# Performance work log

Hardware: AMD Instinct MI355X
Metric: run time of the kernel (lower is better)

Reference implementation:

```python
import jax, jax.numpy as jnp
import numpy as np

N = 30000; E = 480000; B = 32
IN_H = 129; IN_P = 15; HID = 64; HEADS = 8; OUT = 129


def gat_conv(x, src, dst, edge_attr, W, a_src, a_dst, We, a_e, bias, concat):
    # PyG GATConv with edge_dim, add_self_loops=True (fill_value='mean'), negative_slope=0.2
    n = x.shape[0]
    H, C = a_src.shape
    ones = jnp.ones((src.shape[0],), x.dtype)
    deg = jax.ops.segment_sum(ones, dst, num_segments=n)
    ea_mean = jax.ops.segment_sum(edge_attr, dst, num_segments=n) / jnp.clip(deg, 1.0)[:, None]
    loop = jnp.arange(n, dtype=src.dtype)
    s = jnp.concatenate([src, loop])
    t = jnp.concatenate([dst, loop])
    ea = jnp.concatenate([edge_attr, ea_mean], axis=0)
    xw = (x @ W).reshape(n, H, C)              # [N,H,C]
    a_s = jnp.sum(xw * a_src, axis=-1)         # [N,H]
    a_d = jnp.sum(xw * a_dst, axis=-1)         # [N,H]
    ew = (ea @ We).reshape(-1, H, C)           # [E2,H,C]
    a_ed = jnp.sum(ew * a_e, axis=-1)          # [E2,H]
    alpha = jax.nn.leaky_relu(a_s[s] + a_d[t] + a_ed, 0.2)
    amax = jax.ops.segment_max(alpha, t, num_segments=n)   # every node has a self-loop
    expa = jnp.exp(alpha - amax[t])
    denom = jax.ops.segment_sum(expa, t, num_segments=n)
    alpha = expa / denom[t]                    # segment softmax over dst
    out = jax.ops.segment_sum(xw[s] * alpha[..., None], t, num_segments=n)  # [N,H,C]
    out = out.reshape(n, H * C) if concat else jnp.mean(out, axis=1)
    return out + bias


def setup_inputs():
    key = jax.random.key(0)
    ks = jax.random.split(key, 40)
    g = lambda k, s: (jax.random.normal(k, s, jnp.float32) * (1.0 / np.sqrt(s[0])))
    d = {}
    d['x_hrtf'] = jax.random.normal(ks[0], (N, IN_H), jnp.float32)
    d['x_pos'] = jax.random.normal(ks[1], (N, IN_P), jnp.float32)
    d['edge_attr_hrtf'] = jax.random.normal(ks[2], (E, 1), jnp.float32)
    d['edge_attr_pos'] = jax.random.normal(ks[3], (E, 1), jnp.float32)
    # hrtf branch, layer 1 (heads=8, concat)
    d['W1h'] = g(ks[4], (IN_H, HEADS * HID)); d['as1h'] = g(ks[5], (HEADS, HID)); d['ad1h'] = g(ks[6], (HEADS, HID))
    d['We1h'] = g(ks[7], (1, HEADS * HID)); d['ae1h'] = g(ks[8], (HEADS, HID)); d['b1h'] = jnp.zeros((HEADS * HID,), jnp.float32)
    # hrtf branch, layer 2 (heads=1, mean)
    d['W2h'] = g(ks[9], (HEADS * HID, OUT)); d['as2h'] = g(ks[10], (1, OUT)); d['ad2h'] = g(ks[11], (1, OUT))
    d['We2h'] = g(ks[12], (1, OUT)); d['ae2h'] = g(ks[13], (1, OUT)); d['b2h'] = jnp.zeros((OUT,), jnp.float32)
    # pos branch, layer 1
    d['W1p'] = g(ks[14], (IN_P, HEADS * HID)); d['as1p'] = g(ks[15], (HEADS, HID)); d['ad1p'] = g(ks[16], (HEADS, HID))
    d['We1p'] = g(ks[17], (1, HEADS * HID)); d['ae1p'] = g(ks[18], (HEADS, HID)); d['b1p'] = jnp.zeros((HEADS * HID,), jnp.float32)
    # pos branch, layer 2
    d['W2p'] = g(ks[19], (HEADS * HID, OUT)); d['as2p'] = g(ks[20], (1, OUT)); d['ad2p'] = g(ks[21], (1, OUT))
    d['We2p'] = g(ks[22], (1, OUT)); d['ae2p'] = g(ks[23], (1, OUT)); d['b2p'] = jnp.zeros((OUT,), jnp.float32)
    # final fc
    d['Wfc'] = g(ks[24], (2 * OUT, 129)); d['bfc'] = jnp.zeros((129,), jnp.float32)
    d['edge_index_hrtf'] = jax.random.randint(ks[25], (2, E), 0, N, jnp.int32)
    d['edge_index_pos'] = jax.random.randint(ks[26], (2, E), 0, N, jnp.int32)
    d['batch'] = ((jnp.arange(N) * B) // N).astype(jnp.int32)  # sorted, equal-sized graphs
    d['num_graphs'] = B
    return d


def reference(x_hrtf, x_pos, edge_attr_hrtf, edge_attr_pos, W1h, as1h, ad1h, We1h, ae1h, b1h, W2h, as2h, ad2h, We2h, ae2h, b2h, W1p, as1p, ad1p, We1p, ae1p, b1p, W2p, as2p, ad2p, We2p, ae2p, b2p, Wfc, bfc, edge_index_hrtf, edge_index_pos, batch, num_graphs):
    sh, th = edge_index_hrtf[0], edge_index_hrtf[1]
    sp, tp = edge_index_pos[0], edge_index_pos[1]
    h = jax.nn.elu(gat_conv(x_hrtf, sh, th, edge_attr_hrtf, W1h, as1h, ad1h, We1h, ae1h, b1h, True))
    h = gat_conv(h, sh, th, edge_attr_hrtf, W2h, as2h, ad2h, We2h, ae2h, b2h, False)
    p = jax.nn.elu(gat_conv(x_pos, sp, tp, edge_attr_pos, W1p, as1p, ad1p, We1p, ae1p, b1p, True))
    p = gat_conv(p, sp, tp, edge_attr_pos, W2p, as2p, ad2p, We2p, ae2p, b2p, False)
    counts = jax.ops.segment_sum(jnp.ones_like(batch), batch, num_segments=num_graphs)
    last = jnp.cumsum(counts) - 1              # last node index of each graph
    z = jnp.concatenate([h[last], p[last]], axis=-1)
    z = z @ Wfc + bfc
    return z[:, None, :]                       # [B,1,129]
```

## Files before the change

### kernel.cpp

```cpp
#include <hip/hip_runtime.h>

#define N_NODES 30000
#define N_EDGES 480000
#define NB      32
#define HEADS   8
#define F1      512
#define OUT_C   129
#define OUT_S   132
#define W1TS    132

#define CAP1   1024
#define MAXD   64
#define NZREG  (8 + 2 * CAP1 + 2 * NB)

#define SHIFT1 12.0f
#define SHIFT2 20.0f

__device__ __forceinline__ float lrelu(float a) { return a > 0.f ? a : 0.2f * a; }

__device__ __forceinline__ int graph_of(int v) { return (int)(((unsigned)v * 2u) / 1875u); }
__device__ __forceinline__ int last_of(int b) { return (int)((((unsigned)(b + 1) * 1875u) + 1u) / 2u) - 1; }
__device__ __forceinline__ bool is_last_node(int v) { return v == last_of(graph_of(v)); }

__global__ void k_prep(const float* We1h, const float* ae1h,
                       const float* We1p, const float* ae1p,
                       const float* We2h, const float* ae2h,
                       const float* We2p, const float* ae2p,
                       const float* __restrict__ W1h, const float* __restrict__ W1p,
                       const float* as1h, const float* as1p,
                       const float* ad1h, const float* ad1p,
                       float* k12, float* __restrict__ w_as, float* __restrict__ w_ad,
                       int* __restrict__ zreg, int* __restrict__ inv1) {
    int gid = blockIdx.x * 256 + threadIdx.x;
    if (gid < 15000) ((int4*)inv1)[gid] = make_int4(-1, -1, -1, -1);
    if (gid < NZREG) zreg[gid] = 0;
    if (blockIdx.x == 0) {
        int t = threadIdx.x;
        if (t < 8) {
            float s = 0.f;
            for (int c = 0; c < 64; c++) s += We1h[t * 64 + c] * ae1h[t * 64 + c];
            k12[t] = s;
        } else if (t < 16) {
            int h = t - 8;
            float s = 0.f;
            for (int c = 0; c < 64; c++) s += We1p[h * 64 + c] * ae1p[h * 64 + c];
            k12[8 + h] = s;
        } else if (t == 16) {
            float s = 0.f;
            for (int c = 0; c < OUT_C; c++) s += We2h[c] * ae2h[c];
            k12[16] = s;
        } else if (t == 17) {
            float s = 0.f;
            for (int c = 0; c < OUT_C; c++) s += We2p[c] * ae2p[c];
            k12[17] = s;
        }
    }
    if (blockIdx.x >= 64 && blockIdx.x < 96) {
        int bb = blockIdx.x - 64;
        int br = bb >> 4, type = (bb >> 3) & 1, h = bb & 7;
        const float* W1 = br ? W1p : W1h;
        const float* a  = type ? (br ? ad1p : ad1h) : (br ? as1p : as1h);
        float* outp = (type ? w_ad : w_as) + (size_t)(br * 8 + h) * W1TS;
        int K = br ? 15 : 129;
        int d = threadIdx.x;
        if (d < K) {
            float s = 0.f;
            for (int c = 0; c < 64; c++) s += W1[(size_t)d * F1 + h * 64 + c] * a[h * 64 + c];
            outp[d] = s;
        }
    }
}

__global__ __launch_bounds__(256) void k_scan2(const int* __restrict__ ei_h,
        const int* __restrict__ ei_p, const float* __restrict__ ea_h,
        const float* __restrict__ ea_p, int* inv1,
        int* degcnt2, int* eb2v, float* eb2e) {
    int br = blockIdx.y;
    const int* ei = br ? ei_p : ei_h;
    const float* ea = br ? ea_p : ea_h;
    const int* src = ei; const int* dst = ei + N_EDGES;
    inv1 += br * N_NODES;
    degcnt2 += br * NB; eb2v += br * NB * MAXD; eb2e += br * NB * MAXD;
    int tid = threadIdx.x;
    if (blockIdx.x == 0 && tid < NB) inv1[last_of(tid)] = -2;
    int base = (blockIdx.x * 256 + tid) * 4;
    if (base >= N_EDGES) return;
    int4 d = *(const int4*)(dst + base);
    int dv[4] = {d.x, d.y, d.z, d.w};
#pragma unroll
    for (int q = 0; q < 4; q++) {
        if (is_last_node(dv[q])) {
            int e = base + q;
            int b = graph_of(dv[q]);
            int slot = atomicAdd(degcnt2 + b, 1);
            if (slot < MAXD) { eb2v[b * MAXD + slot] = src[e]; eb2e[b * MAXD + slot] = ea[e]; }
            inv1[src[e]] = -2;
        }
    }
}

__global__ __launch_bounds__(256) void k_compact1(int* inv1, int* nodes1, int* cnt) {
    __shared__ int s_v[256];
    __shared__ int s_n, s_base;
    int br = blockIdx.y;
    inv1 += br * N_NODES; nodes1 += br * CAP1;
    int* cntp = cnt + br * 4 + 0;
    int tid = threadIdx.x;
    if (tid == 0) s_n = 0;
    __syncthreads();
    int base = (blockIdx.x * 256 + tid) * 4;
    if (base < N_NODES) {
        int4 w = *(const int4*)(inv1 + base);
        int vv[4] = {w.x, w.y, w.z, w.w};
#pragma unroll
        for (int q = 0; q < 4; q++) {
            if (vv[q] == -2) {
                int p = atomicAdd(&s_n, 1);
                if (p < 256) s_v[p] = base + q;
            }
        }
    }
    __syncthreads();
    int n = s_n; if (n > 256) n = 256;
    if (tid == 0) s_base = atomicAdd(cntp, n);
    __syncthreads();
    for (int q = tid; q < n; q += 256) {
        int j = s_base + q;
        if (j < CAP1) { inv1[s_v[q]] = j; nodes1[j] = s_v[q]; }
    }
}

__global__ __launch_bounds__(256) void k_scan1(const int* __restrict__ ei_h,
        const int* __restrict__ ei_p, const float* __restrict__ ea_h,
        const float* __restrict__ ea_p, const int* __restrict__ inv1,
        int* degcnt1, int* ebv1, float* ebe1) {
    int br = blockIdx.y;
    const int* ei = br ? ei_p : ei_h;
    const float* ea = br ? ea_p : ea_h;
    const int* src = ei; const int* dst = ei + N_EDGES;
    inv1 += br * N_NODES;
    degcnt1 += br * CAP1; ebv1 += (size_t)br * CAP1 * MAXD; ebe1 += (size_t)br * CAP1 * MAXD;
    int tid = threadIdx.x;
    int base = (blockIdx.x * 256 + tid) * 4;
    if (base >= N_EDGES) return;
    int4 d = *(const int4*)(dst + base);
    int dv[4] = {d.x, d.y, d.z, d.w};
#pragma unroll
    for (int q = 0; q < 4; q++) {
        int jj = inv1[dv[q]];
        if (jj >= 0) {
            int e = base + q;
            int slot = atomicAdd(degcnt1 + jj, 1);
            if (slot < MAXD) { ebv1[jj * MAXD + slot] = src[e]; ebe1[jj * MAXD + slot] = ea[e]; }
        }
    }
}

__global__ __launch_bounds__(256) void k_agg1x(const int* __restrict__ ebv1,
        const float* __restrict__ ebe1, const int* __restrict__ degcnt1,
        const int* __restrict__ nodes1, const int* cnt,
        const float* __restrict__ x_h, const float* __restrict__ x_p,
        const float* __restrict__ w_as, const float* __restrict__ w_ad,
        const float* __restrict__ k12, const float* __restrict__ b1h,
        const float* __restrict__ b1p, const float* __restrict__ W1h,
        const float* __restrict__ W1p, const float* __restrict__ W2h,
        const float* __restrict__ W2p, const float* __restrict__ as2h,
        const float* __restrict__ as2p, const float* __restrict__ ad2h,
        const float* __restrict__ ad2p,
        float* __restrict__ xw2, float* __restrict__ as2v, float* __restrict__ ad2all) {
    __shared__ float s_x[MAXD + 9][W1TS];
    __shared__ int   s_v[MAXD + 1];
    __shared__ float s_e[MAXD + 1];
    __shared__ float s_ex[(MAXD + 1) * 8];
    __shared__ float s_den[8];
    __shared__ float s_adh[8];
    __shared__ float s_k1[8];
    __shared__ float s_h1[F1];
    __shared__ float s_row[OUT_S];
    int br = blockIdx.y;
    const float* x    = br ? x_p : x_h;
    const float* b1   = br ? b1p : b1h;
    const float* W1   = br ? W1p : W1h;
    const float* W2   = br ? W2p : W2h;
    const float* as2w = br ? as2p : as2h;
    const float* ad2w = br ? ad2p : ad2h;
    const float* wasb = w_as + (size_t)br * 8 * W1TS;
    const float* wadb = w_ad + (size_t)br * 8 * W1TS;
    int K = br ? 15 : 129;
    int n1 = cnt[br * 4 + 0]; if (n1 > CAP1) n1 = CAP1;
    int j = blockIdx.x;
    if (j >= n1) return;
    int tid = threadIdx.x;
    int deg = degcnt1[br * CAP1 + j]; if (deg > MAXD) deg = MAXD;
    const int*   ebv = ebv1 + ((size_t)br * CAP1 + j) * MAXD;
    const float* ebe = ebe1 + ((size_t)br * CAP1 + j) * MAXD;
    if (tid < deg) { s_v[tid] = ebv[tid]; s_e[tid] = ebe[tid]; }
    if (tid == 0) s_v[deg] = nodes1[br * CAP1 + j];
    if (tid >= 72 && tid < 80) s_k1[tid - 72] = k12[br * 8 + (tid - 72)];
    __syncthreads();
    int total = deg + 1;
    for (int k = tid >> 6; k < total; k += 4) {
        const float* xr = x + (size_t)s_v[k] * K;
        for (int d = (tid & 63); d < K; d += 64) s_x[k][d] = xr[d];
    }
    __syncthreads();
    if (tid < 64) {
        float part = (tid < deg) ? s_e[tid] : 0.f;
#pragma unroll
        for (int o = 32; o > 0; o >>= 1) part += __shfl_down(part, o);
        if (tid == 0) s_e[deg] = part / fmaxf((float)deg, 1.f);
    }
    for (int t = tid; t < total * 8 + 8; t += 256) {
        int k, h; const float* wv;
        if (t < total * 8) { k = t >> 3; h = t & 7; wv = wasb + (size_t)h * W1TS; }
        else               { k = deg; h = t - total * 8; wv = wadb + (size_t)h * W1TS; }
        float dot = 0.f;
        for (int d = 0; d < K; d++) dot += s_x[k][d] * wv[d];
        if (t < total * 8) s_ex[t] = dot; else s_adh[h] = dot;
    }
    __syncthreads();
    for (int t = tid; t < total * 8; t += 256) {
        int k = t >> 3, h = t & 7;
        float a = lrelu(s_ex[t] + s_adh[h] + s_e[k] * s_k1[h]);
        s_ex[t] = __expf(a - SHIFT1);
    }
    __syncthreads();
    if (tid >= 192 && tid < 200) {
        int h = tid - 192;
        float d = 0.f;
        for (int k = 0; k < total; k++) d += s_ex[k * 8 + h];
        s_den[h] = d;
    }
    if (tid < K) {
        float acc[8];
#pragma unroll
        for (int h = 0; h < 8; h++) acc[h] = 0.f;
        for (int k = 0; k < total; k++) {
            float xv = s_x[k][tid];
#pragma unroll
            for (int h = 0; h < 8; h++) acc[h] += s_ex[k * 8 + h] * xv;
        }
#pragma unroll
        for (int h = 0; h < 8; h++) s_x[MAXD + 1 + h][tid] = acc[h];
    }
    __syncthreads();
    {
        int h0 = tid >> 6, h1i = h0 + 4;
        float a0 = 0.f, a1 = 0.f;
        for (int d = 0; d < K; d++) {
            float xa0 = s_x[MAXD + 1 + h0][d];
            float xa1 = s_x[MAXD + 1 + h1i][d];
            a0 += xa0 * W1[(size_t)d * F1 + tid];
            a1 += xa1 * W1[(size_t)d * F1 + tid + 256];
        }
        float v0 = a0 / s_den[h0] + b1[tid];
        float v1 = a1 / s_den[h1i] + b1[tid + 256];
        s_h1[tid]       = v0 > 0.f ? v0 : (__expf(v0) - 1.f);
        s_h1[tid + 256] = v1 > 0.f ? v1 : (__expf(v1) - 1.f);
    }
    __syncthreads();
    if (tid < OUT_C) {
        float a = 0.f;
        for (int k = 0; k < F1; k++) a += s_h1[k] * W2[(size_t)k * OUT_C + tid];
        s_row[tid] = a;
        xw2[((size_t)br * CAP1 + j) * OUT_S + tid] = a;
    }
    __syncthreads();
    if (tid < 128) {
        int w = tid >> 6, l = tid & 63;
        const float* av = w ? ad2w : as2w;
        float p = s_row[l] * av[l] + s_row[64 + l] * av[64 + l];
        if (l == 0) p += s_row[128] * av[128];
#pragma unroll
        for (int o = 32; o > 0; o >>= 1) p += __shfl_down(p, o);
        if (l == 0) {
            if (w) ad2all[br * CAP1 + j] = p;
            else   as2v[br * CAP1 + j] = p;
        }
    }
}

__global__ __launch_bounds__(256) void k_agg2fc(const int* __restrict__ eb2v,
        const float* __restrict__ eb2e, const int* __restrict__ degcnt2,
        const int* __restrict__ inv1, const int* cnt,
        const float* __restrict__ as2v, const float* __restrict__ ad2all,
        const float* __restrict__ k12, const float* __restrict__ b2h,
        const float* __restrict__ b2p, const float* __restrict__ xw2,
        const float* __restrict__ Wfc, const float* __restrict__ bfc,
        float* __restrict__ out) {
    __shared__ int   s_j[MAXD + 1];
    __shared__ float s_e[MAXD + 1];
    __shared__ float s_ex[MAXD + 1];
    __shared__ float s_den;
    __shared__ float hcat[2 * OUT_C];
    int b = blockIdx.x;
    int tid = threadIdx.x;
    for (int br = 0; br < 2; br++) {
        const float* b2 = br ? b2p : b2h;
        const int* inv1b = inv1 + br * N_NODES;
        const float* as2vb = as2v + br * CAP1;
        const float* ad2b = ad2all + br * CAP1;
        const float* xw2b = xw2 + (size_t)br * CAP1 * OUT_S;
        float k2 = k12[16 + br];
        int deg = degcnt2[br * NB + b]; if (deg > MAXD) deg = MAXD;
        if (tid < deg) {
            s_j[tid] = inv1b[eb2v[(br * NB + b) * MAXD + tid]];
            s_e[tid] = eb2e[(br * NB + b) * MAXD + tid];
        }
        if (tid == 0) s_j[deg] = inv1b[last_of(b)];
        __syncthreads();
        if (tid < 64) {
            float part = (tid < deg) ? s_e[tid] : 0.f;
#pragma unroll
            for (int o = 32; o > 0; o >>= 1) part += __shfl_down(part, o);
            if (tid == 0) s_e[deg] = part / fmaxf((float)deg, 1.f);
        }
        __syncthreads();
        int total = deg + 1;
        float adv = ad2b[s_j[deg]];
        for (int k = tid; k < total; k += 256)
            s_ex[k] = __expf(lrelu(as2vb[s_j[k]] + adv + s_e[k] * k2) - SHIFT2);
        __syncthreads();
        if (tid == 0) {
            float d = 0.f;
            for (int k = 0; k < total; k++) d += s_ex[k];
            s_den = d;
        }
        __syncthreads();
        if (tid < OUT_C) {
            float acc = 0.f;
            for (int k = 0; k < total; k++)
                acc += s_ex[k] * xw2b[(size_t)s_j[k] * OUT_S + tid];
            hcat[br * OUT_C + tid] = acc / s_den + b2[tid];
        }
        __syncthreads();
    }
    if (tid < OUT_C) {
        float s = bfc[tid];
        for (int k = 0; k < 2 * OUT_C; k++) s += hcat[k] * Wfc[k * OUT_C + tid];
        out[b * OUT_C + tid] = s;
    }
}

extern "C" void kernel_launch(void* const* d_in, const int* in_sizes, int n_in,
                              void* d_out, int out_size, void* d_ws, size_t ws_size,
                              hipStream_t stream) {
    const float* x_h  = (const float*)d_in[0];
    const float* x_p  = (const float*)d_in[1];
    const float* ea_h = (const float*)d_in[2];
    const float* ea_p = (const float*)d_in[3];
    const float* W1h  = (const float*)d_in[4];
    const float* as1h = (const float*)d_in[5];
    const float* ad1h = (const float*)d_in[6];
    const float* We1h = (const float*)d_in[7];
    const float* ae1h = (const float*)d_in[8];
    const float* b1h  = (const float*)d_in[9];
    const float* W2h  = (const float*)d_in[10];
    const float* as2h = (const float*)d_in[11];
    const float* ad2h = (const float*)d_in[12];
    const float* We2h = (const float*)d_in[13];
    const float* ae2h = (const float*)d_in[14];
    const float* b2h  = (const float*)d_in[15];
    const float* W1p  = (const float*)d_in[16];
    const float* as1p = (const float*)d_in[17];
    const float* ad1p = (const float*)d_in[18];
    const float* We1p = (const float*)d_in[19];
    const float* ae1p = (const float*)d_in[20];
    const float* b1p  = (const float*)d_in[21];
    const float* W2p  = (const float*)d_in[22];
    const float* as2p = (const float*)d_in[23];
    const float* ad2p = (const float*)d_in[24];
    const float* We2p = (const float*)d_in[25];
    const float* ae2p = (const float*)d_in[26];
    const float* b2p  = (const float*)d_in[27];
    const float* Wfc  = (const float*)d_in[28];
    const float* bfc  = (const float*)d_in[29];
    const int*   ei_h = (const int*)d_in[30];
    const int*   ei_p = (const int*)d_in[31];

    char* wsb = (char*)d_ws;
    size_t off = 0;
    auto alloc = [&](size_t elems) -> char* {
        char* p = wsb + off;
        off += ((elems * 4 + 255) / 256) * 256;
        return p;
    };
    float*    k12     = (float*)alloc(18);
    int*      zreg    = (int*)alloc(NZREG);
    int*      cnt     = zreg;
    int*      degcnt1 = zreg + 8;
    int*      degcnt2 = zreg + 8 + 2 * CAP1;
    int*      inv1    = (int*)alloc(2 * N_NODES);
    int*      nodes1  = (int*)alloc(2 * CAP1);
    int*      ebv1    = (int*)alloc(2 * (size_t)CAP1 * MAXD);
    float*    ebe1    = (float*)alloc(2 * (size_t)CAP1 * MAXD);
    int*      eb2v    = (int*)alloc(2 * NB * MAXD);
    float*    eb2e    = (float*)alloc(2 * NB * MAXD);
    float*    w_as    = (float*)alloc(2 * 8 * W1TS);
    float*    w_ad    = (float*)alloc(2 * 8 * W1TS);
    float*    xw2     = (float*)alloc(2 * (size_t)CAP1 * OUT_S);
    float*    as2v    = (float*)alloc(2 * CAP1);
    float*    ad2all  = (float*)alloc(2 * CAP1);
    if (off > ws_size) return;

    const int EBLK4 = (N_EDGES / 4 + 255) / 256;
    const int NBLK4 = (N_NODES / 4 + 255) / 256;

    k_prep<<<96, 256, 0, stream>>>(
        We1h, ae1h, We1p, ae1p, We2h, ae2h, We2p, ae2p,
        W1h, W1p, as1h, as1p, ad1h, ad1p,
        k12, w_as, w_ad, zreg, inv1);
    k_scan2<<<dim3(EBLK4, 2), 256, 0, stream>>>(ei_h, ei_p, ea_h, ea_p, inv1,
                                                degcnt2, eb2v, eb2e);
    k_compact1<<<dim3(NBLK4, 2), 256, 0, stream>>>(inv1, nodes1, cnt);
    k_scan1<<<dim3(EBLK4, 2), 256, 0, stream>>>(ei_h, ei_p, ea_h, ea_p, inv1,
                                                degcnt1, ebv1, ebe1);
    k_agg1x<<<dim3(CAP1, 2), 256, 0, stream>>>(ebv1, ebe1, degcnt1, nodes1, cnt,
                                               x_h, x_p, w_as, w_ad, k12, b1h, b1p,
                                               W1h, W1p, W2h, W2p, as2h, as2p, ad2h, ad2p,
                                               xw2, as2v, ad2all);
    k_agg2fc<<<NB, 256, 0, stream>>>(eb2v, eb2e, degcnt2, inv1, cnt,
                                     as2v, ad2all, k12, b2h, b2p, xw2, Wfc, bfc, (float*)d_out);
}
```

Baseline: 90.51 us.

## Fuse node compaction into edge scan via atomic claims, fold prep into scan1

Removes the separate compaction kernel. Nodes are claimed with atomicCAS during the last-node edge scan and given compact indices through per-block shared buffers plus a global counter. The weight-precompute work (attention-folded W1 columns and edge constants) moves into extra blocks of the second edge scan, and zero-init becomes a small standalone kernel. This cuts launches and a full pass over inv1, at the cost of more global atomics and a nondeterministic compaction order.

```diff
diff --git a/kernel.cpp b/kernel.cpp
--- a/kernel.cpp
+++ b/kernel.cpp
@@ -17,138 +17,139 @@
 #define SHIFT2 20.0f
 
 __device__ __forceinline__ float lrelu(float a) { return a > 0.f ? a : 0.2f * a; }
+__device__ __forceinline__ float elu1(float v) { return v > 0.f ? v : (__expf(v) - 1.f); }
 
 __device__ __forceinline__ int graph_of(int v) { return (int)(((unsigned)v * 2u) / 1875u); }
 __device__ __forceinline__ int last_of(int b) { return (int)((((unsigned)(b + 1) * 1875u) + 1u) / 2u) - 1; }
 __device__ __forceinline__ bool is_last_node(int v) { return v == last_of(graph_of(v)); }
 
-__global__ void k_prep(const float* We1h, const float* ae1h,
-                       const float* We1p, const float* ae1p,
-                       const float* We2h, const float* ae2h,
-                       const float* We2p, const float* ae2p,
-                       const float* __restrict__ W1h, const float* __restrict__ W1p,
-                       const float* as1h, const float* as1p,
-                       const float* ad1h, const float* ad1p,
-                       float* k12, float* __restrict__ w_as, float* __restrict__ w_ad,
-                       int* __restrict__ zreg, int* __restrict__ inv1) {
+__global__ void k_init(int* __restrict__ zreg, int* __restrict__ inv1) {
     int gid = blockIdx.x * 256 + threadIdx.x;
     if (gid < 15000) ((int4*)inv1)[gid] = make_int4(-1, -1, -1, -1);
     if (gid < NZREG) zreg[gid] = 0;
-    if (blockIdx.x == 0) {
-        int t = threadIdx.x;
-        if (t < 8) {
-            float s = 0.f;
-            for (int c = 0; c < 64; c++) s += We1h[t * 64 + c] * ae1h[t * 64 + c];
-            k12[t] = s;
-        } else if (t < 16) {
-            int h = t - 8;
-            float s = 0.f;
-            for (int c = 0; c < 64; c++) s += We1p[h * 64 + c] * ae1p[h * 64 + c];
-            k12[8 + h] = s;
-        } else if (t == 16) {
-            float s = 0.f;
-            for (int c = 0; c < OUT_C; c++) s += We2h[c] * ae2h[c];
-            k12[16] = s;
-        } else if (t == 17) {
-            float s = 0.f;
-            for (int c = 0; c < OUT_C; c++) s += We2p[c] * ae2p[c];
-            k12[17] = s;
-        }
-    }
-    if (blockIdx.x >= 64 && blockIdx.x < 96) {
-        int bb = blockIdx.x - 64;
-        int br = bb >> 4, type = (bb >> 3) & 1, h = bb & 7;
-        const float* W1 = br ? W1p : W1h;
-        const float* a  = type ? (br ? ad1p : ad1h) : (br ? as1p : as1h);
-        float* outp = (type ? w_ad : w_as) + (size_t)(br * 8 + h) * W1TS;
-        int K = br ? 15 : 129;
-        int d = threadIdx.x;
-        if (d < K) {
-            float s = 0.f;
-            for (int c = 0; c < 64; c++) s += W1[(size_t)d * F1 + h * 64 + c] * a[h * 64 + c];
-            outp[d] = s;
-        }
-    }
-}
-
-__global__ __launch_bounds__(256) void k_scan2(const int* __restrict__ ei_h,
+}
+
+__global__ __launch_bounds__(256) void k_scan2c(const int* __restrict__ ei_h,
         const int* __restrict__ ei_p, const float* __restrict__ ea_h,
-        const float* __restrict__ ea_p, int* inv1,
+        const float* __restrict__ ea_p, int* inv1, int* nodes1, int* cnt,
         int* degcnt2, int* eb2v, float* eb2e) {
+    __shared__ int s_claim[128];
+    __shared__ int s_n, s_base;
     int br = blockIdx.y;
     const int* ei = br ? ei_p : ei_h;
     const float* ea = br ? ea_p : ea_h;
     const int* src = ei; const int* dst = ei + N_EDGES;
-    inv1 += br * N_NODES;
-    degcnt2 += br * NB; eb2v += br * NB * MAXD; eb2e += br * NB * MAXD;
+    int* inv1b = inv1 + br * N_NODES;
+    int* nodes1b = nodes1 + br * CAP1;
+    int* cntp = cnt + br * 4;
+    int* dc2 = degcnt2 + br * NB;
+    int* e2v = eb2v + br * NB * MAXD;
+    float* e2e = eb2e + br * NB * MAXD;
     int tid = threadIdx.x;
-    if (blockIdx.x == 0 && tid < NB) inv1[last_of(tid)] = -2;
+    if (tid == 0) s_n = 0;
+    __syncthreads();
+    auto claim = [&](int v) {
+        if (atomicCAS(&inv1b[v], -1, -3) == -1) {
+            int p = atomicAdd(&s_n, 1);
+            if (p < 128) s_claim[p] = v;
+            else {
+                int j = atomicAdd(cntp, 1);
+                if (j < CAP1) { nodes1b[j] = v; inv1b[v] = j; }
+                else inv1b[v] = -1;
+            }
+        }
+    };
+    if (blockIdx.x == 0 && tid < NB) claim(last_of(tid));
     int base = (blockIdx.x * 256 + tid) * 4;
+    if (base < N_EDGES) {
+        int4 d4 = *(const int4*)(dst + base);
+        int dv[4] = {d4.x, d4.y, d4.z, d4.w};
+#pragma unroll
+        for (int q = 0; q < 4; q++) {
+            if (is_last_node(dv[q])) {
+                int e = base + q;
+                int b = graph_of(dv[q]);
+                int slot = atomicAdd(dc2 + b, 1);
+                if (slot < MAXD) { e2v[b * MAXD + slot] = src[e]; e2e[b * MAXD + slot] = ea[e]; }
+                claim(src[e]);
+            }
+        }
+    }
+    __syncthreads();
+    int n = s_n; if (n > 128) n = 128;
+    if (tid == 0) s_base = atomicAdd(cntp, n);
+    __syncthreads();
+    for (int q = tid; q < n; q += 256) {
+        int j = s_base + q;
+        int v = s_claim[q];
+        if (j < CAP1) { nodes1b[j] = v; inv1b[v] = j; }
+        else inv1b[v] = -1;
+    }
+}
+
+__global__ __launch_bounds__(256) void k_scan1w(const int* __restrict__ ei_h,
+        const int* __restrict__ ei_p, const float* __restrict__ ea_h,
+        const float* __restrict__ ea_p, const int* __restrict__ inv1,
+        int* degcnt1, int* ebv1, float* ebe1,
+        const float* __restrict__ W1h, const float* __restrict__ W1p,
+        const float* as1h, const float* as1p,
+        const float* ad1h, const float* ad1p,
+        const float* We1h, const float* ae1h, const float* We1p, const float* ae1p,
+        const float* We2h, const float* ae2h, const float* We2p, const float* ae2p,
+        float* __restrict__ w_as, float* __restrict__ w_ad, float* __restrict__ k12) {
+    const int EBLK4 = (N_EDGES / 4 + 255) / 256;
+    int br = blockIdx.y;
+    int chunk = blockIdx.x;
+    int tid = threadIdx.x;
+    if (chunk >= EBLK4) {
+        int ex = chunk - EBLK4;
+        if (ex < 16) {
+            int type = ex >> 3, h = ex & 7;
+            const float* W1 = br ? W1p : W1h;
+            const float* a  = type ? (br ? ad1p : ad1h) : (br ? as1p : as1h);
+            float* outp = (type ? w_ad : w_as) + (size_t)(br * 8 + h) * W1TS;
+            int K = br ? 15 : 129;
+            if (tid < K) {
+                float s = 0.f;
+                for (int c = 0; c < 64; c++) s += W1[(size_t)tid * F1 + h * 64 + c] * a[h * 64 + c];
+                outp[tid] = s;
+            }
+        } else if (br == 0) {
+            int t = tid;
+            if (t < 8) {
+                float s = 0.f;
+                for (int c = 0; c < 64; c++) s += We1h[t * 64 + c] * ae1h[t * 64 + c];
+                k12[t] = s;
+            } else if (t < 16) {
+                int h = t - 8;
+                float s = 0.f;
+                for (int c = 0; c < 64; c++) s += We1p[h * 64 + c] * ae1p[h * 64 + c];
+                k12[8 + h] = s;
+            } else if (t == 16) {
+                float s = 0.f;
+                for (int c = 0; c < OUT_C; c++) s += We2h[c] * ae2h[c];
+                k12[16] = s;
+            } else if (t == 17) {
+                float s = 0.f;
+                for (int c = 0; c < OUT_C; c++) s += We2p[c] * ae2p[c];
+                k12[17] = s;
+            }
+        }
+        return;
+    }
+    const int* ei = br ? ei_p : ei_h;
+    const float* ea = br ? ea_p : ea_h;
+    const int* src = ei; const int* dst = ei + N_EDGES;
+    const int* inv1b = inv1 + br * N_NODES;
+    degcnt1 += br * CAP1; ebv1 += (size_t)br * CAP1 * MAXD; ebe1 += (size_t)br * CAP1 * MAXD;
+    int base = (chunk * 256 + tid) * 4;
     if (base >= N_EDGES) return;
     int4 d = *(const int4*)(dst + base);
     int dv[4] = {d.x, d.y, d.z, d.w};
 #pragma unroll
     for (int q = 0; q < 4; q++) {
-        if (is_last_node(dv[q])) {
-            int e = base + q;
-            int b = graph_of(dv[q]);
-            int slot = atomicAdd(degcnt2 + b, 1);
-            if (slot < MAXD) { eb2v[b * MAXD + slot] = src[e]; eb2e[b * MAXD + slot] = ea[e]; }
-            inv1[src[e]] = -2;
-        }
-    }
-}
-
-__global__ __launch_bounds__(256) void k_compact1(int* inv1, int* nodes1, int* cnt) {
-    __shared__ int s_v[256];
-    __shared__ int s_n, s_base;
-    int br = blockIdx.y;
-    inv1 += br * N_NODES; nodes1 += br * CAP1;
-    int* cntp = cnt + br * 4 + 0;
-    int tid = threadIdx.x;
-    if (tid == 0) s_n = 0;
-    __syncthreads();
-    int base = (blockIdx.x * 256 + tid) * 4;
-    if (base < N_NODES) {
-        int4 w = *(const int4*)(inv1 + base);
-        int vv[4] = {w.x, w.y, w.z, w.w};
-#pragma unroll
-        for (int q = 0; q < 4; q++) {
-            if (vv[q] == -2) {
-                int p = atomicAdd(&s_n, 1);
-                if (p < 256) s_v[p] = base + q;
-            }
-        }
-    }
-    __syncthreads();
-    int n = s_n; if (n > 256) n = 256;
-    if (tid == 0) s_base = atomicAdd(cntp, n);
-    __syncthreads();
-    for (int q = tid; q < n; q += 256) {
-        int j = s_base + q;
-        if (j < CAP1) { inv1[s_v[q]] = j; nodes1[j] = s_v[q]; }
-    }
-}
-
-__global__ __launch_bounds__(256) void k_scan1(const int* __restrict__ ei_h,
-        const int* __restrict__ ei_p, const float* __restrict__ ea_h,
-        const float* __restrict__ ea_p, const int* __restrict__ inv1,
-        int* degcnt1, int* ebv1, float* ebe1) {
-    int br = blockIdx.y;
-    const int* ei = br ? ei_p : ei_h;
-    const float* ea = br ? ea_p : ea_h;
-    const int* src = ei; const int* dst = ei + N_EDGES;
-    inv1 += br * N_NODES;
-    degcnt1 += br * CAP1; ebv1 += (size_t)br * CAP1 * MAXD; ebe1 += (size_t)br * CAP1 * MAXD;
-    int tid = threadIdx.x;
-    int base = (blockIdx.x * 256 + tid) * 4;
-    if (base >= N_EDGES) return;
-    int4 d = *(const int4*)(dst + base);
-    int dv[4] = {d.x, d.y, d.z, d.w};
-#pragma unroll
-    for (int q = 0; q < 4; q++) {
-        int jj = inv1[dv[q]];
-        if (jj >= 0) {
+        int jj = inv1b[dv[q]];
+        if (jj >= 0 && jj < CAP1) {
             int e = base + q;
             int slot = atomicAdd(degcnt1 + jj, 1);
             if (slot < MAXD) { ebv1[jj * MAXD + slot] = src[e]; ebe1[jj * MAXD + slot] = ea[e]; }
@@ -255,8 +256,8 @@
         }
         float v0 = a0 / s_den[h0] + b1[tid];
         float v1 = a1 / s_den[h1i] + b1[tid + 256];
-        s_h1[tid]       = v0 > 0.f ? v0 : (__expf(v0) - 1.f);
-        s_h1[tid + 256] = v1 > 0.f ? v1 : (__expf(v1) - 1.f);
+        s_h1[tid]       = elu1(v0);
+        s_h1[tid + 256] = elu1(v1);
     }
     __syncthreads();
     if (tid < OUT_C) {
@@ -404,17 +405,16 @@
     if (off > ws_size) return;
 
     const int EBLK4 = (N_EDGES / 4 + 255) / 256;
-    const int NBLK4 = (N_NODES / 4 + 255) / 256;
-
-    k_prep<<<96, 256, 0, stream>>>(
-        We1h, ae1h, We1p, ae1p, We2h, ae2h, We2p, ae2p,
-        W1h, W1p, as1h, as1p, ad1h, ad1p,
-        k12, w_as, w_ad, zreg, inv1);
-    k_scan2<<<dim3(EBLK4, 2), 256, 0, stream>>>(ei_h, ei_p, ea_h, ea_p, inv1,
-                                                degcnt2, eb2v, eb2e);
-    k_compact1<<<dim3(NBLK4, 2), 256, 0, stream>>>(inv1, nodes1, cnt);
-    k_scan1<<<dim3(EBLK4, 2), 256, 0, stream>>>(ei_h, ei_p, ea_h, ea_p, inv1,
-                                                degcnt1, ebv1, ebe1);
+
+    k_init<<<59, 256, 0, stream>>>(zreg, inv1);
+    k_scan2c<<<dim3(EBLK4, 2), 256, 0, stream>>>(ei_h, ei_p, ea_h, ea_p, inv1,
+                                                 nodes1, cnt, degcnt2, eb2v, eb2e);
+    k_scan1w<<<dim3(EBLK4 + 17, 2), 256, 0, stream>>>(ei_h, ei_p, ea_h, ea_p, inv1,
+                                                      degcnt1, ebv1, ebe1,
+                                                      W1h, W1p, as1h, as1p, ad1h, ad1p,
+                                                      We1h, ae1h, We1p, ae1p,
+                                                      We2h, ae2h, We2p, ae2p,
+                                                      w_as, w_ad, k12);
     k_agg1x<<<dim3(CAP1, 2), 256, 0, stream>>>(ebv1, ebe1, degcnt1, nodes1, cnt,
                                                x_h, x_p, w_as, w_ad, k12, b1h, b1p,
                                                W1h, W1p, W2h, W2p, as2h, as2p, ad2h, ad2p,
```

Result: slower. 96.08 us (+6.1%).
